# Optimization experiments

Measured on AMD Instinct MI355X. Metric: run time of the kernel, lower is better.

The kernel has to match this reference:

```python
import jax, jax.numpy as jnp
import numpy as np

B, C, H, W = 16, 512, 64, 64
SCALE = 8
CQK = C // SCALE  # 64
EPS = 1e-6


def setup_inputs() -> dict:
    key = jax.random.key(0)
    ks = jax.random.split(key, 8)
    x = jax.random.normal(ks[0], (B, C, H, W), dtype=jnp.float32)
    # 1x1 conv weights stored as [out_ch, in_ch] (kernel_size=1)
    Wq = jax.random.normal(ks[1], (CQK, C), dtype=jnp.float32) * 0.02
    bq = jnp.zeros((CQK,), dtype=jnp.float32)
    Wk = jax.random.normal(ks[2], (CQK, C), dtype=jnp.float32) * 0.02
    bk = jnp.zeros((CQK,), dtype=jnp.float32)
    Wv = jax.random.normal(ks[3], (C, C), dtype=jnp.float32) * 0.02
    bv = jnp.zeros((C,), dtype=jnp.float32)
    # gamma is initialized to 0 in the module; use a nonzero value so the
    # output is non-trivial for kernel correctness checks.
    gamma = jax.random.normal(ks[4], (1,), dtype=jnp.float32)
    return {"x": x, "Wq": Wq, "bq": bq, "Wk": Wk, "bk": bk,
            "Wv": Wv, "bv": bv, "gamma": gamma}


def _l2norm_ch(t):
    # normalize over the channel axis (dim=-2), matching torch.norm(p=2, dim=-2)
    nrm = jnp.sqrt(jnp.sum(t * t, axis=-2, keepdims=True))
    return t / jnp.maximum(nrm, EPS)


def reference(x, Wq, bq, Wk, bk, Wv, bv, gamma):
    b, c, h, w = x.shape
    n = h * w
    xf = x.reshape(b, c, n)                                   # [B,C,N]
    # 1x1 convs == channel matmuls
    Q = jnp.einsum('oc,bcn->bon', Wq, xf) + bq[None, :, None]  # [B,cqk,N]
    K = jnp.einsum('oc,bcn->bon', Wk, xf) + bk[None, :, None]  # [B,cqk,N]
    V = jnp.einsum('oc,bcn->bon', Wv, xf) + bv[None, :, None]  # [B,C,N]
    Qn = _l2norm_ch(Q).transpose(0, 2, 1)                      # [B,N,cqk]
    Kn = _l2norm_ch(K)                                         # [B,cqk,N]
    # Taylor-softmax surrogate denominator
    denom = n + jnp.einsum('bnc,bc->bn', Qn, Kn.sum(axis=-1))  # [B,N]
    tailor = 1.0 / jnp.maximum(denom, 1e-6)                    # [B,N]
    # KtV accumulation: [B,cqk,C]
    matrix = jnp.einsum('bmn,bcn->bmc', Kn, V)
    value_sum = jnp.sum(V, axis=-1)[:, :, None]                # [B,C,1] -> broadcast
    matrix_sum = value_sum + jnp.einsum('bnm,bmc->bcn', Qn, matrix)  # [B,C,N]
    weight_value = matrix_sum * tailor[:, None, :]             # [B,C,N]
    out = gamma * weight_value.reshape(b, c, h, w)
    return jnp.nan_to_num(out, nan=0.0, posinf=1.0, neginf=-1.0)
```

## Files before the change

kernel.cpp:

```cpp
#include <hip/hip_runtime.h>


typedef __attribute__((ext_vector_type(8))) short short8_t;
typedef __attribute__((ext_vector_type(4))) float f32x4;

__device__ __forceinline__ unsigned short f2bf(float f) {
  union { float f; unsigned u; } v; v.f = f;
  unsigned r = v.u + 0x7FFFu + ((v.u >> 16) & 1u);
  return (unsigned short)(r >> 16);
}
__device__ __forceinline__ float bf2f(unsigned short h) {
  union { unsigned u; float f; } v; v.u = ((unsigned)h) << 16;
  return v.f;
}

#define MFMA(a, b, c) __builtin_amdgcn_mfma_f32_16x16x32_bf16((a), (b), (c), 0, 0, 0)

__global__ void k_prep(const float* __restrict__ Wq, const float* __restrict__ Wk,
                       unsigned short* __restrict__ Wqk) {
  int idx = blockIdx.x * 256 + threadIdx.x;
  int o = idx >> 9, c = idx & 511;
  float v = (o < 64) ? Wq[o * 512 + c] : Wk[(o - 64) * 512 + c];
  Wqk[idx] = f2bf(v);
}

__launch_bounds__(256, 2)
__global__ void k_qk(const float* __restrict__ x, const unsigned short* __restrict__ Wqk,
                     const float* __restrict__ bq, const float* __restrict__ bk,
                     unsigned short* __restrict__ QnT, unsigned short* __restrict__ KnG,
                     float* __restrict__ Ksum) {
  __shared__ __align__(16) unsigned char smem[77312];
  unsigned short* SAb[2] = {(unsigned short*)(smem + 0),
                            (unsigned short*)(smem + 18432)};
  unsigned short* SBb[2] = {(unsigned short*)(smem + 36864),
                            (unsigned short*)(smem + 55296)};
  unsigned short* EQ = (unsigned short*)(smem + 0);
  unsigned short* EK = (unsigned short*)(smem + 18432);
  float* ssq   = (float*)(smem + 73728);
  float* invq  = (float*)(smem + 75776);
  float* invk  = (float*)(smem + 76288);
  float* biasL = (float*)(smem + 76800);

  const int t = threadIdx.x;
  const int lane = t & 63, w = t >> 6;
  const int l15 = lane & 15, quad = lane >> 4;
  const int nt = blockIdx.x, b = blockIdx.y;
  const int n0 = nt * 128;
  const float* xb = x + (size_t)b * 512 * 4096;

  if (t < 128) biasL[t] = (t < 64) ? bq[t] : bk[t - 64];

  f32x4 acc[2][8];
#pragma unroll
  for (int i = 0; i < 2; ++i)
#pragma unroll
    for (int j = 0; j < 8; ++j) acc[i][j] = (f32x4){0.f, 0.f, 0.f, 0.f};

  const int nB = t & 127;
  const int cgB = t >> 7;
  const float* bsrc0 = xb + (size_t)(cgB * 32) * 4096 + n0 + nB;

  short8_t apre[4];
  float bpre[32];

#define QK_LOADA(kc_) do {                                                     \
    const int c0_ = (kc_) * 64;                                                \
    _Pragma("unroll")                                                          \
    for (int p = 0; p < 4; ++p) {                                              \
      int gid = t + p * 256; int o_ = gid >> 3, cg = gid & 7;                  \
      apre[p] = *(const short8_t*)(Wqk + o_ * 512 + c0_ + cg * 8);             \
    } } while (0)

#define QK_LOADB(kc_) do {                                                     \
    const float* s_ = bsrc0 + (size_t)(kc_) * 64 * 4096;                       \
    _Pragma("unroll")                                                          \
    for (int i = 0; i < 32; ++i) bpre[i] = s_[(size_t)i * 4096];               \
    } while (0)

#define QK_STORE(pb) do {                                                      \
    unsigned short* SAp = SAb[pb]; unsigned short* SBp = SBb[pb];              \
    _Pragma("unroll")                                                          \
    for (int p = 0; p < 4; ++p) {                                              \
      int gid = t + p * 256; int o_ = gid >> 3, cg = gid & 7;                  \
      *(short8_t*)(SAp + o_ * 72 + cg * 8) = apre[p];                          \
    }                                                                          \
    _Pragma("unroll")                                                          \
    for (int j = 0; j < 4; ++j) {                                              \
      short8_t v_;                                                             \
      _Pragma("unroll")                                                        \
      for (int e = 0; e < 8; ++e) v_[e] = (short)f2bf(bpre[j * 8 + e]);        \
      *(short8_t*)(SBp + nB * 72 + cgB * 32 + j * 8) = v_;                     \
    } } while (0)

#define QK_MM(pb) do {                                                         \
    const unsigned short* SAp = SAb[pb]; const unsigned short* SBp = SBb[pb];  \
    _Pragma("unroll")                                                          \
    for (int s = 0; s < 2; ++s) {                                              \
      short8_t a0 = *(const short8_t*)(SAp + (w * 32 + l15) * 72 + s * 32 + quad * 8);      \
      short8_t a1 = *(const short8_t*)(SAp + (w * 32 + 16 + l15) * 72 + s * 32 + quad * 8); \
      _Pragma("unroll")                                                        \
      for (int tc = 0; tc < 8; ++tc) {                                         \
        short8_t bf_ = *(const short8_t*)(SBp + (tc * 16 + l15) * 72 + s * 32 + quad * 8);  \
        acc[0][tc] = MFMA(a0, bf_, acc[0][tc]);                                \
        acc[1][tc] = MFMA(a1, bf_, acc[1][tc]);                                \
      } } } while (0)

  QK_LOADA(0); QK_LOADB(0);
#pragma unroll
  for (int kc = 0; kc < 8; ++kc) {
    const int pb = kc & 1;
    QK_STORE(pb);
    if (kc < 7) { QK_LOADA(kc + 1); QK_LOADB(kc + 1); }
    __syncthreads();
    QK_MM(pb);
  }
  __syncthreads();

#pragma unroll
  for (int trl = 0; trl < 2; ++trl)
#pragma unroll
    for (int reg = 0; reg < 4; ++reg) {
      int o = w * 32 + trl * 16 + quad * 4 + reg;
      float bias = biasL[o];
#pragma unroll
      for (int tc = 0; tc < 8; ++tc) acc[trl][tc][reg] += bias;
    }

#pragma unroll
  for (int tc = 0; tc < 8; ++tc) {
    float v = 0.f;
#pragma unroll
    for (int trl = 0; trl < 2; ++trl)
#pragma unroll
      for (int reg = 0; reg < 4; ++reg) {
        float q = acc[trl][tc][reg];
        v += q * q;
      }
    v += __shfl_xor(v, 16);
    v += __shfl_xor(v, 32);
    if (quad == 0) ssq[w * 128 + tc * 16 + l15] = v;
  }
  __syncthreads();
  if (t < 128) {
    float qs = ssq[t] + ssq[128 + t];
    float ks = ssq[256 + t] + ssq[384 + t];
    invq[t] = 1.0f / fmaxf(sqrtf(qs), 1e-6f);
    invk[t] = 1.0f / fmaxf(sqrtf(ks), 1e-6f);
  }
  __syncthreads();

  if (w < 2) {
#pragma unroll
    for (int trl = 0; trl < 2; ++trl)
#pragma unroll
      for (int tc = 0; tc < 8; ++tc) {
        int n = tc * 16 + l15;
        float inv = invq[n];
#pragma unroll
        for (int reg = 0; reg < 4; ++reg) {
          int o = w * 32 + trl * 16 + quad * 4 + reg;
          EQ[n * 72 + o] = f2bf(acc[trl][tc][reg] * inv);
        }
      }
  } else {
#pragma unroll
    for (int trl = 0; trl < 2; ++trl)
#pragma unroll
      for (int reg = 0; reg < 4; ++reg) {
        int m = (w - 2) * 32 + trl * 16 + quad * 4 + reg;
        float p = 0.f;
#pragma unroll
        for (int tc = 0; tc < 8; ++tc) {
          int n = tc * 16 + l15;
          float val = acc[trl][tc][reg] * invk[n];
          EK[m * 136 + n] = f2bf(val);
          p += val;
        }
        p += __shfl_xor(p, 1);
        p += __shfl_xor(p, 2);
        p += __shfl_xor(p, 4);
        p += __shfl_xor(p, 8);
        if (l15 == 0) atomicAdd(Ksum + b * 64 + m, p);
      }
  }
  __syncthreads();

  unsigned short* qdst = QnT + ((size_t)b * 4096 + n0) * 64;
#pragma unroll
  for (int p = 0; p < 4; ++p) {
    int idx = t + p * 256;
    int row = idx >> 3, seg = idx & 7;
    *(short8_t*)(qdst + row * 64 + seg * 8) = *(const short8_t*)(EQ + row * 72 + seg * 8);
  }
  unsigned short* kdst = KnG + (size_t)b * 64 * 4096 + n0;
#pragma unroll
  for (int p = 0; p < 4; ++p) {
    int idx = t + p * 256;
    int row = idx >> 4, seg = idx & 15;
    *(short8_t*)(kdst + (size_t)row * 4096 + seg * 8) =
        *(const short8_t*)(EK + row * 136 + seg * 8);
  }
#undef QK_LOADA
#undef QK_LOADB
#undef QK_STORE
#undef QK_MM
}

__launch_bounds__(256, 2)
__global__ void k_t(const float* __restrict__ x, const unsigned short* __restrict__ KnG,
                    float* __restrict__ T, float* __restrict__ xsum) {
  __shared__ __align__(16) unsigned char smem[55296];
  unsigned short* SAb[2] = {(unsigned short*)(smem + 0),
                            (unsigned short*)(smem + 9216)};
  unsigned short* SBb[2] = {(unsigned short*)(smem + 18432),
                            (unsigned short*)(smem + 36864)};
  const int t = threadIdx.x;
  const int lane = t & 63, w = t >> 6;
  const int l15 = lane & 15, quad = lane >> 4;
  const int ns = blockIdx.x, ct = blockIdx.y, b = blockIdx.z;
  const int c0 = ct * 128;
  const float* xb = x + (size_t)b * 512 * 4096;
  const unsigned short* Knb = KnG + (size_t)b * 64 * 4096 + ns * 512;

  f32x4 acc[4][2];
#pragma unroll
  for (int i = 0; i < 4; ++i)
#pragma unroll
    for (int j = 0; j < 2; ++j) acc[i][j] = (f32x4){0.f, 0.f, 0.f, 0.f};

  const int row = t >> 1, half = t & 1;
  float xs = 0.f;
  const float* bbase = xb + (size_t)(c0 + row) * 4096 + ns * 512 + half * 32;

  short8_t apre[2];
  f32x4 bpre[8];

#define T_LOADA(ch_) do {                                                      \
    _Pragma("unroll")                                                          \
    for (int p = 0; p < 2; ++p) {                                              \
      int gid = t + p * 256; int m_ = gid >> 3, cg = gid & 7;                  \
      apre[p] = *(const short8_t*)(Knb + (size_t)m_ * 4096 + (ch_) * 64 + cg * 8); \
    } } while (0)

#define T_LOADB(ch_) do {                                                      \
    const float* s_ = bbase + (ch_) * 64;                                      \
    _Pragma("unroll")                                                          \
    for (int q = 0; q < 8; ++q) bpre[q] = *(const f32x4*)(s_ + q * 4);         \
    } while (0)

#define T_STORE(pb) do {                                                       \
    unsigned short* SAp = SAb[pb]; unsigned short* SBp = SBb[pb];              \
    _Pragma("unroll")                                                          \
    for (int p = 0; p < 2; ++p) {                                              \
      int gid = t + p * 256; int m_ = gid >> 3, cg = gid & 7;                  \
      *(short8_t*)(SAp + m_ * 72 + cg * 8) = apre[p];                          \
    }                                                                          \
    _Pragma("unroll")                                                          \
    for (int j = 0; j < 4; ++j) {                                              \
      short8_t v_;                                                             \
      _Pragma("unroll")                                                        \
      for (int e = 0; e < 4; ++e) {                                            \
        float f0 = bpre[j * 2][e], f1 = bpre[j * 2 + 1][e];                    \
        xs += f0 + f1;                                                         \
        v_[e] = (short)f2bf(f0); v_[4 + e] = (short)f2bf(f1);                  \
      }                                                                        \
      *(short8_t*)(SBp + row * 72 + half * 32 + j * 8) = v_;                   \
    } } while (0)

#define T_MM(pb) do {                                                          \
    const unsigned short* SAp = SAb[pb]; const unsigned short* SBp = SBb[pb];  \
    _Pragma("unroll")                                                          \
    for (int s = 0; s < 2; ++s) {                                              \
      short8_t af[4];                                                          \
      _Pragma("unroll")                                                        \
      for (int tm = 0; tm < 4; ++tm)                                           \
        af[tm] = *(const short8_t*)(SAp + (tm * 16 + l15) * 72 + s * 32 + quad * 8); \
      _Pragma("unroll")                                                        \
      for (int tcl = 0; tcl < 2; ++tcl) {                                      \
        short8_t bf_ = *(const short8_t*)(SBp + (w * 32 + tcl * 16 + l15) * 72 + s * 32 + quad * 8); \
        _Pragma("unroll")                                                      \
        for (int tm = 0; tm < 4; ++tm) acc[tm][tcl] = MFMA(af[tm], bf_, acc[tm][tcl]); \
      } } } while (0)

  T_LOADA(0); T_LOADB(0);
#pragma unroll
  for (int ch = 0; ch < 8; ++ch) {
    const int pb = ch & 1;
    T_STORE(pb);
    if (ch < 7) { T_LOADA(ch + 1); T_LOADB(ch + 1); }
    __syncthreads();
    T_MM(pb);
  }

  xs += __shfl_xor(xs, 1);
  if (half == 0) atomicAdd(xsum + b * 512 + c0 + row, xs);
#pragma unroll
  for (int tm = 0; tm < 4; ++tm)
#pragma unroll
    for (int tcl = 0; tcl < 2; ++tcl)
#pragma unroll
      for (int reg = 0; reg < 4; ++reg) {
        int m = tm * 16 + quad * 4 + reg;
        int c = c0 + w * 32 + tcl * 16 + l15;
        atomicAdd(T + ((size_t)b * 64 + m) * 512 + c, acc[tm][tcl][reg]);
      }
#undef T_LOADA
#undef T_LOADB
#undef T_STORE
#undef T_MM
}

__launch_bounds__(256, 2)
__global__ void k_mat(const float* __restrict__ T, const float* __restrict__ Wv,
                      const float* __restrict__ bv, const float* __restrict__ xsum,
                      const float* __restrict__ Ksum,
                      unsigned short* __restrict__ matT, float* __restrict__ Vsum) {
  __shared__ __align__(16) unsigned char smem[27136];
  float* ST = (float*)smem;
  float* SW = (float*)(smem + 17408);
  float* SV = (float*)(smem + 26112);
  const int t = threadIdx.x;
  const int cb = blockIdx.x, b = blockIdx.y;
  const int c0 = cb * 32;
  const int m = t >> 2, cs = t & 3;
  float acc[8] = {0.f, 0.f, 0.f, 0.f, 0.f, 0.f, 0.f, 0.f};

  for (int kc = 0; kc < 8; ++kc) {
    __syncthreads();
#pragma unroll
    for (int p = 0; p < 4; ++p) {
      int idx = t + p * 256;
      int row = idx >> 4, f4 = idx & 15;
      *(f32x4*)(ST + row * 68 + f4 * 4) =
          *(const f32x4*)(T + ((size_t)b * 64 + row) * 512 + kc * 64 + f4 * 4);
    }
#pragma unroll
    for (int p = 0; p < 2; ++p) {
      int idx = t + p * 256;
      int row = idx >> 4, f4 = idx & 15;
      *(f32x4*)(SW + row * 68 + f4 * 4) =
          *(const f32x4*)(Wv + (size_t)(c0 + row) * 512 + kc * 64 + f4 * 4);
    }
    __syncthreads();
    for (int kk = 0; kk < 64; ++kk) {
      float tv = ST[m * 68 + kk];
#pragma unroll
      for (int j = 0; j < 8; ++j) acc[j] += tv * SW[(cs + j * 4) * 68 + kk];
    }
  }
  float ks = Ksum[b * 64 + m];
#pragma unroll
  for (int j = 0; j < 8; ++j) {
    int c = c0 + cs + j * 4;
    float mv = acc[j] + bv[c] * ks;
    matT[((size_t)b * 512 + c) * 64 + m] = f2bf(mv);
  }
  {
    int cc = t >> 3, kp = t & 7;
    const float* wr = Wv + (size_t)(c0 + cc) * 512 + kp * 64;
    const float* xr = xsum + b * 512 + kp * 64;
    float s = 0.f;
    for (int i = 0; i < 64; ++i) s += wr[i] * xr[i];
    SV[cc * 8 + kp] = s;
  }
  __syncthreads();
  if (t < 32) {
    float s = 0.f;
#pragma unroll
    for (int i = 0; i < 8; ++i) s += SV[t * 8 + i];
    int c = c0 + t;
    Vsum[b * 512 + c] = s + 4096.0f * bv[c];
  }
}

__launch_bounds__(256, 2)
__global__ void k_out(const unsigned short* __restrict__ QnT,
                      const unsigned short* __restrict__ matT,
                      const float* __restrict__ Ksum, const float* __restrict__ Vsum,
                      const float* __restrict__ gamma, float* __restrict__ out) {
  __shared__ __align__(16) unsigned char smem[38144];
  unsigned short* SA = (unsigned short*)smem;
  unsigned short* SB = (unsigned short*)(smem + 18432);
  float* Ksl  = (float*)(smem + 36864);
  float* tail = (float*)(smem + 37120);
  float* vs   = (float*)(smem + 37632);
  const int t = threadIdx.x;
  const int lane = t & 63, w = t >> 6;
  const int l15 = lane & 15, quad = lane >> 4;
  const int nt = blockIdx.x, ct = blockIdx.y, b = blockIdx.z;
  const int n0 = nt * 128, c0 = ct * 128;

  const unsigned short* asrc = matT + ((size_t)b * 512 + c0) * 64;
  const unsigned short* bsrc = QnT + ((size_t)b * 4096 + n0) * 64;
#pragma unroll
  for (int p = 0; p < 4; ++p) {
    int idx = t + p * 256;
    int row = idx >> 3, seg = idx & 7;
    *(short8_t*)(SA + row * 72 + seg * 8) = *(const short8_t*)(asrc + row * 64 + seg * 8);
    *(short8_t*)(SB + row * 72 + seg * 8) = *(const short8_t*)(bsrc + row * 64 + seg * 8);
  }
  if (t < 64) Ksl[t] = Ksum[b * 64 + t];
  if (t >= 128) vs[t - 128] = Vsum[b * 512 + c0 + (t - 128)];
  __syncthreads();
  if (t < 128) {
    float d = 0.f;
#pragma unroll
    for (int mm = 0; mm < 64; ++mm) d += bf2f(SB[t * 72 + mm]) * Ksl[mm];
    tail[t] = 1.0f / fmaxf(4096.0f + d, 1e-6f);
  }

  f32x4 acc[2][8];
#pragma unroll
  for (int i = 0; i < 2; ++i)
#pragma unroll
    for (int j = 0; j < 8; ++j) acc[i][j] = (f32x4){0.f, 0.f, 0.f, 0.f};

#pragma unroll
  for (int s = 0; s < 2; ++s) {
    short8_t a0 = *(const short8_t*)(SA + (w * 32 + l15) * 72 + s * 32 + quad * 8);
    short8_t a1 = *(const short8_t*)(SA + (w * 32 + 16 + l15) * 72 + s * 32 + quad * 8);
#pragma unroll
    for (int tc = 0; tc < 8; ++tc) {
      short8_t bfr = *(const short8_t*)(SB + (tc * 16 + l15) * 72 + s * 32 + quad * 8);
      acc[0][tc] = MFMA(a0, bfr, acc[0][tc]);
      acc[1][tc] = MFMA(a1, bfr, acc[1][tc]);
    }
  }
  __syncthreads();
  const float g = gamma[0];
  float* ob = out + (size_t)b * 512 * 4096;
#pragma unroll
  for (int trl = 0; trl < 2; ++trl)
#pragma unroll
    for (int tc = 0; tc < 8; ++tc) {
      int n = tc * 16 + l15;
      float tl = tail[n] * g;
#pragma unroll
      for (int reg = 0; reg < 4; ++reg) {
        int cl = w * 32 + trl * 16 + quad * 4 + reg;
        float val = tl * (vs[cl] + acc[trl][tc][reg]);
        ob[(size_t)(c0 + cl) * 4096 + n0 + n] = val;
      }
    }
}

extern "C" void kernel_launch(void* const* d_in, const int* in_sizes, int n_in,
                              void* d_out, int out_size, void* d_ws, size_t ws_size,
                              hipStream_t stream) {
  const float* x     = (const float*)d_in[0];
  const float* Wq    = (const float*)d_in[1];
  const float* bq    = (const float*)d_in[2];
  const float* Wk    = (const float*)d_in[3];
  const float* bk    = (const float*)d_in[4];
  const float* Wv    = (const float*)d_in[5];
  const float* bv    = (const float*)d_in[6];
  const float* gamma = (const float*)d_in[7];
  float* out = (float*)d_out;
  char* ws = (char*)d_ws;

  float* T    = (float*)(ws + 0);
  float* xsum = (float*)(ws + 2097152);
  float* Ksum = (float*)(ws + 2129920);
  float* Vsum = (float*)(ws + 2134016);
  unsigned short* Wqk  = (unsigned short*)(ws + 2166784);
  unsigned short* matT = (unsigned short*)(ws + 2297856);
  unsigned short* QnT  = (unsigned short*)(ws + 3346432);
  unsigned short* Kn   = (unsigned short*)(ws + 11735040);

  hipMemsetAsync(ws, 0, 2134016, stream);
  k_prep<<<256, 256, 0, stream>>>(Wq, Wk, Wqk);
  k_qk<<<dim3(32, 16), 256, 0, stream>>>(x, Wqk, bq, bk, QnT, Kn, Ksum);
  k_t<<<dim3(8, 4, 16), 256, 0, stream>>>(x, Kn, T, xsum);
  k_mat<<<dim3(16, 16), 256, 0, stream>>>(T, Wv, bv, xsum, Ksum, matT, Vsum);
  k_out<<<dim3(32, 4, 16), 256, 0, stream>>>(QnT, matT, Ksum, Vsum, gamma, out);
}
```

Measured before the change: 322.9 us.

## Load MFMA A-fragments directly, replace T atomics with partials, stage output stores

k_qk and k_t now load the weight/Kn A-operand fragments straight from global memory into registers, double-buffered, instead of staging them through LDS. This shrinks shared memory and drops LDS round trips. k_t writes per-split partial T tiles instead of issuing float atomicAdds, and k_mat sums the eight partials when loading, which removes most of the memset. k_out stages results through LDS so it can emit coalesced float4 output stores, and it vectorizes the denominator dot product. The cost is more registers, extra workspace traffic for the partials, and uncoalesced per-lane global A loads.

```diff
diff --git a/kernel.cpp b/kernel.cpp
--- a/kernel.cpp
+++ b/kernel.cpp
@@ -29,17 +29,15 @@
                      const float* __restrict__ bq, const float* __restrict__ bk,
                      unsigned short* __restrict__ QnT, unsigned short* __restrict__ KnG,
                      float* __restrict__ Ksum) {
-  __shared__ __align__(16) unsigned char smem[77312];
-  unsigned short* SAb[2] = {(unsigned short*)(smem + 0),
+  __shared__ __align__(16) unsigned char smem[40448];
+  unsigned short* SBb[2] = {(unsigned short*)(smem + 0),
                             (unsigned short*)(smem + 18432)};
-  unsigned short* SBb[2] = {(unsigned short*)(smem + 36864),
-                            (unsigned short*)(smem + 55296)};
   unsigned short* EQ = (unsigned short*)(smem + 0);
   unsigned short* EK = (unsigned short*)(smem + 18432);
-  float* ssq   = (float*)(smem + 73728);
-  float* invq  = (float*)(smem + 75776);
-  float* invk  = (float*)(smem + 76288);
-  float* biasL = (float*)(smem + 76800);
+  float* ssq   = (float*)(smem + 36864);
+  float* invq  = (float*)(smem + 38912);
+  float* invk  = (float*)(smem + 39424);
+  float* biasL = (float*)(smem + 39936);
 
   const int t = threadIdx.x;
   const int lane = t & 63, w = t >> 6;
@@ -59,16 +57,17 @@
   const int nB = t & 127;
   const int cgB = t >> 7;
   const float* bsrc0 = xb + (size_t)(cgB * 32) * 4096 + n0 + nB;
-
-  short8_t apre[4];
+  const unsigned short* arow0 = Wqk + (w * 32 + l15) * 512 + quad * 8;
+  const unsigned short* arow1 = arow0 + 16 * 512;
+
   float bpre[32];
-
-#define QK_LOADA(kc_) do {                                                     \
-    const int c0_ = (kc_) * 64;                                                \
-    _Pragma("unroll")                                                          \
-    for (int p = 0; p < 4; ++p) {                                              \
-      int gid = t + p * 256; int o_ = gid >> 3, cg = gid & 7;                  \
-      apre[p] = *(const short8_t*)(Wqk + o_ * 512 + c0_ + cg * 8);             \
+  short8_t apre[2][4];
+
+#define QK_LOADA(kc_, pb_) do {                                                \
+    _Pragma("unroll")                                                          \
+    for (int s = 0; s < 2; ++s) {                                              \
+      apre[pb_][s * 2 + 0] = *(const short8_t*)(arow0 + (kc_) * 64 + s * 32);  \
+      apre[pb_][s * 2 + 1] = *(const short8_t*)(arow1 + (kc_) * 64 + s * 32);  \
     } } while (0)
 
 #define QK_LOADB(kc_) do {                                                     \
@@ -77,13 +76,8 @@
     for (int i = 0; i < 32; ++i) bpre[i] = s_[(size_t)i * 4096];               \
     } while (0)
 
-#define QK_STORE(pb) do {                                                      \
-    unsigned short* SAp = SAb[pb]; unsigned short* SBp = SBb[pb];              \
-    _Pragma("unroll")                                                          \
-    for (int p = 0; p < 4; ++p) {                                              \
-      int gid = t + p * 256; int o_ = gid >> 3, cg = gid & 7;                  \
-      *(short8_t*)(SAp + o_ * 72 + cg * 8) = apre[p];                          \
-    }                                                                          \
+#define QK_STOREB(pb) do {                                                     \
+    unsigned short* SBp = SBb[pb];                                             \
     _Pragma("unroll")                                                          \
     for (int j = 0; j < 4; ++j) {                                              \
       short8_t v_;                                                             \
@@ -93,11 +87,11 @@
     } } while (0)
 
 #define QK_MM(pb) do {                                                         \
-    const unsigned short* SAp = SAb[pb]; const unsigned short* SBp = SBb[pb];  \
+    const unsigned short* SBp = SBb[pb];                                       \
     _Pragma("unroll")                                                          \
     for (int s = 0; s < 2; ++s) {                                              \
-      short8_t a0 = *(const short8_t*)(SAp + (w * 32 + l15) * 72 + s * 32 + quad * 8);      \
-      short8_t a1 = *(const short8_t*)(SAp + (w * 32 + 16 + l15) * 72 + s * 32 + quad * 8); \
+      short8_t a0 = apre[pb][s * 2 + 0];                                       \
+      short8_t a1 = apre[pb][s * 2 + 1];                                       \
       _Pragma("unroll")                                                        \
       for (int tc = 0; tc < 8; ++tc) {                                         \
         short8_t bf_ = *(const short8_t*)(SBp + (tc * 16 + l15) * 72 + s * 32 + quad * 8);  \
@@ -105,12 +99,12 @@
         acc[1][tc] = MFMA(a1, bf_, acc[1][tc]);                                \
       } } } while (0)
 
-  QK_LOADA(0); QK_LOADB(0);
+  QK_LOADB(0); QK_LOADA(0, 0);
 #pragma unroll
   for (int kc = 0; kc < 8; ++kc) {
     const int pb = kc & 1;
-    QK_STORE(pb);
-    if (kc < 7) { QK_LOADA(kc + 1); QK_LOADB(kc + 1); }
+    QK_STOREB(pb);
+    if (kc < 7) { QK_LOADB(kc + 1); QK_LOADA(kc + 1, pb ^ 1); }
     __syncthreads();
     QK_MM(pb);
   }
@@ -202,25 +196,23 @@
   }
 #undef QK_LOADA
 #undef QK_LOADB
-#undef QK_STORE
+#undef QK_STOREB
 #undef QK_MM
 }
 
 __launch_bounds__(256, 2)
 __global__ void k_t(const float* __restrict__ x, const unsigned short* __restrict__ KnG,
-                    float* __restrict__ T, float* __restrict__ xsum) {
-  __shared__ __align__(16) unsigned char smem[55296];
-  unsigned short* SAb[2] = {(unsigned short*)(smem + 0),
-                            (unsigned short*)(smem + 9216)};
-  unsigned short* SBb[2] = {(unsigned short*)(smem + 18432),
-                            (unsigned short*)(smem + 36864)};
+                    float* __restrict__ Tpart, float* __restrict__ xsum) {
+  __shared__ __align__(16) unsigned char smem[36864];
+  unsigned short* SBb[2] = {(unsigned short*)(smem + 0),
+                            (unsigned short*)(smem + 18432)};
   const int t = threadIdx.x;
   const int lane = t & 63, w = t >> 6;
   const int l15 = lane & 15, quad = lane >> 4;
   const int ns = blockIdx.x, ct = blockIdx.y, b = blockIdx.z;
   const int c0 = ct * 128;
   const float* xb = x + (size_t)b * 512 * 4096;
-  const unsigned short* Knb = KnG + (size_t)b * 64 * 4096 + ns * 512;
+  const unsigned short* Knb = KnG + (size_t)b * 64 * 4096 + ns * 512 + quad * 8;
 
   f32x4 acc[4][2];
 #pragma unroll
@@ -232,15 +224,17 @@
   float xs = 0.f;
   const float* bbase = xb + (size_t)(c0 + row) * 4096 + ns * 512 + half * 32;
 
-  short8_t apre[2];
   f32x4 bpre[8];
-
-#define T_LOADA(ch_) do {                                                      \
-    _Pragma("unroll")                                                          \
-    for (int p = 0; p < 2; ++p) {                                              \
-      int gid = t + p * 256; int m_ = gid >> 3, cg = gid & 7;                  \
-      apre[p] = *(const short8_t*)(Knb + (size_t)m_ * 4096 + (ch_) * 64 + cg * 8); \
-    } } while (0)
+  short8_t apre[2][8];
+
+#define T_LOADA(ch_, pb_) do {                                                 \
+    _Pragma("unroll")                                                          \
+    for (int tm = 0; tm < 4; ++tm)                                             \
+      _Pragma("unroll")                                                        \
+      for (int s = 0; s < 2; ++s)                                              \
+        apre[pb_][tm * 2 + s] =                                                \
+            *(const short8_t*)(Knb + (size_t)(tm * 16 + l15) * 4096 + (ch_) * 64 + s * 32); \
+    } while (0)
 
 #define T_LOADB(ch_) do {                                                      \
     const float* s_ = bbase + (ch_) * 64;                                      \
@@ -248,13 +242,8 @@
     for (int q = 0; q < 8; ++q) bpre[q] = *(const f32x4*)(s_ + q * 4);         \
     } while (0)
 
-#define T_STORE(pb) do {                                                       \
-    unsigned short* SAp = SAb[pb]; unsigned short* SBp = SBb[pb];              \
-    _Pragma("unroll")                                                          \
-    for (int p = 0; p < 2; ++p) {                                              \
-      int gid = t + p * 256; int m_ = gid >> 3, cg = gid & 7;                  \
-      *(short8_t*)(SAp + m_ * 72 + cg * 8) = apre[p];                          \
-    }                                                                          \
+#define T_STOREB(pb) do {                                                      \
+    unsigned short* SBp = SBb[pb];                                             \
     _Pragma("unroll")                                                          \
     for (int j = 0; j < 4; ++j) {                                              \
       short8_t v_;                                                             \
@@ -268,32 +257,30 @@
     } } while (0)
 
 #define T_MM(pb) do {                                                          \
-    const unsigned short* SAp = SAb[pb]; const unsigned short* SBp = SBb[pb];  \
+    const unsigned short* SBp = SBb[pb];                                       \
     _Pragma("unroll")                                                          \
     for (int s = 0; s < 2; ++s) {                                              \
-      short8_t af[4];                                                          \
-      _Pragma("unroll")                                                        \
-      for (int tm = 0; tm < 4; ++tm)                                           \
-        af[tm] = *(const short8_t*)(SAp + (tm * 16 + l15) * 72 + s * 32 + quad * 8); \
       _Pragma("unroll")                                                        \
       for (int tcl = 0; tcl < 2; ++tcl) {                                      \
         short8_t bf_ = *(const short8_t*)(SBp + (w * 32 + tcl * 16 + l15) * 72 + s * 32 + quad * 8); \
         _Pragma("unroll")                                                      \
-        for (int tm = 0; tm < 4; ++tm) acc[tm][tcl] = MFMA(af[tm], bf_, acc[tm][tcl]); \
+        for (int tm = 0; tm < 4; ++tm)                                         \
+          acc[tm][tcl] = MFMA(apre[pb][tm * 2 + s], bf_, acc[tm][tcl]);        \
       } } } while (0)
 
-  T_LOADA(0); T_LOADB(0);
+  T_LOADB(0); T_LOADA(0, 0);
 #pragma unroll
   for (int ch = 0; ch < 8; ++ch) {
     const int pb = ch & 1;
-    T_STORE(pb);
-    if (ch < 7) { T_LOADA(ch + 1); T_LOADB(ch + 1); }
+    T_STOREB(pb);
+    if (ch < 7) { T_LOADB(ch + 1); T_LOADA(ch + 1, pb ^ 1); }
     __syncthreads();
     T_MM(pb);
   }
 
   xs += __shfl_xor(xs, 1);
   if (half == 0) atomicAdd(xsum + b * 512 + c0 + row, xs);
+  float* tp = Tpart + ((size_t)b * 8 + ns) * 64 * 512;
 #pragma unroll
   for (int tm = 0; tm < 4; ++tm)
 #pragma unroll
@@ -302,16 +289,16 @@
       for (int reg = 0; reg < 4; ++reg) {
         int m = tm * 16 + quad * 4 + reg;
         int c = c0 + w * 32 + tcl * 16 + l15;
-        atomicAdd(T + ((size_t)b * 64 + m) * 512 + c, acc[tm][tcl][reg]);
+        tp[(size_t)m * 512 + c] = acc[tm][tcl][reg];
       }
 #undef T_LOADA
 #undef T_LOADB
-#undef T_STORE
+#undef T_STOREB
 #undef T_MM
 }
 
 __launch_bounds__(256, 2)
-__global__ void k_mat(const float* __restrict__ T, const float* __restrict__ Wv,
+__global__ void k_mat(const float* __restrict__ Tpart, const float* __restrict__ Wv,
                       const float* __restrict__ bv, const float* __restrict__ xsum,
                       const float* __restrict__ Ksum,
                       unsigned short* __restrict__ matT, float* __restrict__ Vsum) {
@@ -323,16 +310,25 @@
   const int cb = blockIdx.x, b = blockIdx.y;
   const int c0 = cb * 32;
   const int m = t >> 2, cs = t & 3;
+  const float* Tb = Tpart + (size_t)b * 8 * 64 * 512;
   float acc[8] = {0.f, 0.f, 0.f, 0.f, 0.f, 0.f, 0.f, 0.f};
 
   for (int kc = 0; kc < 8; ++kc) {
     __syncthreads();
+#pragma unroll
+    for (int p = 0; p < 1; ++p) {
+      int idx = t;
+      (void)idx;
+    }
 #pragma unroll
     for (int p = 0; p < 4; ++p) {
       int idx = t + p * 256;
       int row = idx >> 4, f4 = idx & 15;
-      *(f32x4*)(ST + row * 68 + f4 * 4) =
-          *(const f32x4*)(T + ((size_t)b * 64 + row) * 512 + kc * 64 + f4 * 4);
+      f32x4 s = (f32x4){0.f, 0.f, 0.f, 0.f};
+#pragma unroll
+      for (int ns = 0; ns < 8; ++ns)
+        s += *(const f32x4*)(Tb + ((size_t)ns * 64 + row) * 512 + kc * 64 + f4 * 4);
+      *(f32x4*)(ST + row * 68 + f4 * 4) = s;
     }
 #pragma unroll
     for (int p = 0; p < 2; ++p) {
@@ -381,6 +377,7 @@
   __shared__ __align__(16) unsigned char smem[38144];
   unsigned short* SA = (unsigned short*)smem;
   unsigned short* SB = (unsigned short*)(smem + 18432);
+  float* EO   = (float*)smem;
   float* Ksl  = (float*)(smem + 36864);
   float* tail = (float*)(smem + 37120);
   float* vs   = (float*)(smem + 37632);
@@ -405,7 +402,11 @@
   if (t < 128) {
     float d = 0.f;
 #pragma unroll
-    for (int mm = 0; mm < 64; ++mm) d += bf2f(SB[t * 72 + mm]) * Ksl[mm];
+    for (int g8 = 0; g8 < 8; ++g8) {
+      short8_t q8 = *(const short8_t*)(SB + t * 72 + g8 * 8);
+#pragma unroll
+      for (int e = 0; e < 8; ++e) d += bf2f((unsigned short)q8[e]) * Ksl[g8 * 8 + e];
+    }
     tail[t] = 1.0f / fmaxf(4096.0f + d, 1e-6f);
   }
 
@@ -426,22 +427,34 @@
       acc[1][tc] = MFMA(a1, bfr, acc[1][tc]);
     }
   }
-  __syncthreads();
+
   const float g = gamma[0];
-  float* ob = out + (size_t)b * 512 * 4096;
-#pragma unroll
-  for (int trl = 0; trl < 2; ++trl)
-#pragma unroll
-    for (int tc = 0; tc < 8; ++tc) {
-      int n = tc * 16 + l15;
-      float tl = tail[n] * g;
-#pragma unroll
-      for (int reg = 0; reg < 4; ++reg) {
-        int cl = w * 32 + trl * 16 + quad * 4 + reg;
-        float val = tl * (vs[cl] + acc[trl][tc][reg]);
-        ob[(size_t)(c0 + cl) * 4096 + n0 + n] = val;
+  float* ob = out + (size_t)b * 512 * 4096 + (size_t)c0 * 4096 + n0;
+#pragma unroll
+  for (int p = 0; p < 2; ++p) {
+    __syncthreads();
+#pragma unroll
+    for (int trl = 0; trl < 2; ++trl)
+#pragma unroll
+      for (int tcs = 0; tcs < 4; ++tcs) {
+        int tc = p * 4 + tcs;
+        int n = tc * 16 + l15;
+        float tl = tail[n] * g;
+#pragma unroll
+        for (int reg = 0; reg < 4; ++reg) {
+          int cl = w * 32 + trl * 16 + quad * 4 + reg;
+          EO[cl * 68 + tcs * 16 + l15] = tl * (vs[cl] + acc[trl][tc][reg]);
+        }
       }
-    }
+    __syncthreads();
+#pragma unroll
+    for (int p2 = 0; p2 < 8; ++p2) {
+      int gid = t + p2 * 256;
+      int row = gid >> 4, f4 = gid & 15;
+      *(f32x4*)(ob + (size_t)row * 4096 + p * 64 + f4 * 4) =
+          *(const f32x4*)(EO + row * 68 + f4 * 4);
+    }
+  }
 }
 
 extern "C" void kernel_launch(void* const* d_in, const int* in_sizes, int n_in,
@@ -458,19 +471,19 @@
   float* out = (float*)d_out;
   char* ws = (char*)d_ws;
 
-  float* T    = (float*)(ws + 0);
-  float* xsum = (float*)(ws + 2097152);
-  float* Ksum = (float*)(ws + 2129920);
-  float* Vsum = (float*)(ws + 2134016);
-  unsigned short* Wqk  = (unsigned short*)(ws + 2166784);
-  unsigned short* matT = (unsigned short*)(ws + 2297856);
-  unsigned short* QnT  = (unsigned short*)(ws + 3346432);
-  unsigned short* Kn   = (unsigned short*)(ws + 11735040);
-
-  hipMemsetAsync(ws, 0, 2134016, stream);
+  float* Tpart = (float*)(ws + 0);
+  float* xsum  = (float*)(ws + 16777216);
+  float* Ksum  = (float*)(ws + 16809984);
+  float* Vsum  = (float*)(ws + 16814080);
+  unsigned short* Wqk  = (unsigned short*)(ws + 16846848);
+  unsigned short* matT = (unsigned short*)(ws + 16977920);
+  unsigned short* QnT  = (unsigned short*)(ws + 18026496);
+  unsigned short* Kn   = (unsigned short*)(ws + 26415104);
+
+  hipMemsetAsync(ws + 16777216, 0, 36864, stream);
   k_prep<<<256, 256, 0, stream>>>(Wq, Wk, Wqk);
   k_qk<<<dim3(32, 16), 256, 0, stream>>>(x, Wqk, bq, bk, QnT, Kn, Ksum);
-  k_t<<<dim3(8, 4, 16), 256, 0, stream>>>(x, Kn, T, xsum);
-  k_mat<<<dim3(16, 16), 256, 0, stream>>>(T, Wv, bv, xsum, Ksum, matT, Vsum);
+  k_t<<<dim3(8, 4, 16), 256, 0, stream>>>(x, Kn, Tpart, xsum);
+  k_mat<<<dim3(16, 16), 256, 0, stream>>>(Tpart, Wv, bv, xsum, Ksum, matT, Vsum);
   k_out<<<dim3(32, 4, 16), 256, 0, stream>>>(QnT, matT, Ksum, Vsum, gamma, out);
 }
```

After: 335.1 us. +3.8%, slower.
